# Performance work log

Hardware: AMD Instinct MI355X
Metric: run time of the kernel (lower is better)

The kernel has to match this reference:

```python
import jax, jax.numpy as jnp
import numpy as np

DIM, D_STATE, D_CONV, EXPAND = 1024, 16, 4, 2
D_INNER = EXPAND * DIM
DT_RANK = (DIM + 15) // 16  # 64
B, L = 2, 1024


def setup_inputs() -> dict:
    key = jax.random.key(0)
    ks = jax.random.split(key, 12)
    s = lambda k, shp, sc: jax.random.normal(k, shp, jnp.float32) * sc
    return {
        "x": s(ks[0], (B, L, DIM), 1.0),
        "ln_g": jnp.ones((DIM,), jnp.float32),
        "ln_b": jnp.zeros((DIM,), jnp.float32),
        "W_in": s(ks[1], (DIM, 2 * D_INNER), DIM ** -0.5),
        "conv_w": s(ks[2], (D_INNER, D_CONV), D_CONV ** -0.5),
        "conv_b": jnp.zeros((D_INNER,), jnp.float32),
        "W_x": s(ks[3], (D_INNER, DT_RANK + 2 * D_STATE), D_INNER ** -0.5),
        "W_dt": s(ks[4], (DT_RANK, D_INNER), DT_RANK ** -0.5),
        "b_dt": s(ks[5], (D_INNER,), 0.1),
        "A_log": jnp.log(jnp.broadcast_to(jnp.arange(1, D_STATE + 1, dtype=jnp.float32), (D_INNER, D_STATE))),
        "D_skip": jnp.ones((D_INNER,), jnp.float32),
        "W_out": s(ks[6], (D_INNER, DIM), D_INNER ** -0.5),
    }


def _mamba_block(x, ln_g, ln_b, W_in, conv_w, conv_b, W_x, W_dt, b_dt, A_log, D_skip, W_out):
    # LayerNorm over feature dim
    mu = jnp.mean(x, -1, keepdims=True)
    var = jnp.mean(jnp.square(x - mu), -1, keepdims=True)
    xn = (x - mu) * jax.lax.rsqrt(var + 1e-5) * ln_g + ln_b

    # in_proj -> (u, z), each (B, L, E)
    u, z = jnp.split(xn @ W_in, 2, axis=-1)

    # causal depthwise conv1d over L (kernel D_CONV) + SiLU
    up = jnp.pad(u, ((0, 0), (D_CONV - 1, 0), (0, 0)))
    uc = conv_b
    for k in range(D_CONV):
        uc = uc + conv_w[:, k] * up[:, k:k + L, :]
    uc = jax.nn.silu(uc)

    # input-dependent dt, B, C
    dbl = uc @ W_x
    dt = jax.nn.softplus(dbl[..., :DT_RANK] @ W_dt + b_dt)      # (B,L,E)
    Bc = dbl[..., DT_RANK:DT_RANK + D_STATE]                    # (B,L,N)
    Cc = dbl[..., DT_RANK + D_STATE:]                           # (B,L,N)

    A = -jnp.exp(A_log)                                         # (E,N)
    dA = jnp.exp(dt[..., None] * A)                             # (B,L,E,N)
    dBu = (dt * uc)[..., None] * Bc[:, :, None, :]              # (B,L,E,N)

    # selective scan: h_t = dA_t * h_{t-1} + dBu_t  (associative)
    def comb(c1, c2):
        a1, b1 = c1
        a2, b2 = c2
        return a2 * a1, a2 * b1 + b2

    _, h = jax.lax.associative_scan(comb, (dA, dBu), axis=1)

    y = jnp.einsum('blen,bln->ble', h, Cc) + uc * D_skip
    y = y * jax.nn.silu(z)
    return y @ W_out                                            # (B,L,DIM)


def reference(x, ln_g, ln_b, W_in, conv_w, conv_b, W_x, W_dt, b_dt, A_log, D_skip, W_out):
    return _mamba_block(x, ln_g, ln_b, W_in, conv_w, conv_b, W_x, W_dt, b_dt, A_log, D_skip, W_out)
```

## Files before the change

kernel.cpp:

```cpp
#include <hip/hip_runtime.h>
#include <hip/hip_bf16.h>

typedef __attribute__((ext_vector_type(4))) float  f32x4;
typedef __attribute__((ext_vector_type(8))) __bf16 bf16x8;

typedef __attribute__((address_space(1))) void gvoid_t;
typedef __attribute__((address_space(3))) void lvoid_t;

__device__ __forceinline__ void gld16(const void* g, void* l) {
    __builtin_amdgcn_global_load_lds((const gvoid_t*)g, (lvoid_t*)l, 16, 0, 0);
}

template <int N> __device__ __forceinline__ void vwait() {
    if constexpr (N == 0)      asm volatile("s_waitcnt vmcnt(0)" ::: "memory");
    else if constexpr (N == 6) asm volatile("s_waitcnt vmcnt(6)" ::: "memory");
    else if constexpr (N == 8) asm volatile("s_waitcnt vmcnt(8)" ::: "memory");
}

__device__ __forceinline__ unsigned short f2bf(float f) {
    unsigned u = __builtin_bit_cast(unsigned, f);
    u += 0x7fffu + ((u >> 16) & 1u);
    return (unsigned short)(u >> 16);
}

__device__ __forceinline__ float silu(float x) {
    return x / (1.f + __expf(-x));
}

__global__ __launch_bounds__(256) void k_transpose_cvt(const float* __restrict__ in,
                                                       unsigned short* __restrict__ out,
                                                       int K, int N, int Npad) {
    __shared__ float t[32][33];
    int bn = blockIdx.x * 32;
    int bk = blockIdx.y * 32;
    int c = threadIdx.x & 31, r0 = threadIdx.x >> 5;
    #pragma unroll
    for (int rr = r0; rr < 32; rr += 8) {
        int k = bk + rr, n = bn + c;
        t[rr][c] = (k < K && n < N) ? in[(size_t)k * N + n] : 0.f;
    }
    __syncthreads();
    #pragma unroll
    for (int rr = r0; rr < 32; rr += 8) {
        int n = bn + rr, k = bk + c;
        if (n < Npad && k < K) out[(size_t)n * K + k] = f2bf(t[c][rr]);
    }
}

__global__ __launch_bounds__(256) void k_ln(const float* __restrict__ x,
                                            const float* __restrict__ g,
                                            const float* __restrict__ b,
                                            unsigned short* __restrict__ xn) {
    int row = blockIdx.x;
    const float4* xr = (const float4*)(x + (size_t)row * 1024);
    float4 v = xr[threadIdx.x];
    float s  = v.x + v.y + v.z + v.w;
    float ss = v.x*v.x + v.y*v.y + v.z*v.z + v.w*v.w;
    #pragma unroll
    for (int o = 32; o > 0; o >>= 1) { s += __shfl_down(s, o); ss += __shfl_down(ss, o); }
    __shared__ float red[8];
    if ((threadIdx.x & 63) == 0) { red[threadIdx.x >> 6] = s; red[4 + (threadIdx.x >> 6)] = ss; }
    __syncthreads();
    s  = red[0] + red[1] + red[2] + red[3];
    ss = red[4] + red[5] + red[6] + red[7];
    float mu  = s * (1.f / 1024.f);
    float inv = rsqrtf(ss * (1.f / 1024.f) - mu * mu + 1e-5f);
    float4 gv = ((const float4*)g)[threadIdx.x];
    float4 bv = ((const float4*)b)[threadIdx.x];
    ushort4 o4;
    o4.x = f2bf((v.x - mu) * inv * gv.x + bv.x);
    o4.y = f2bf((v.y - mu) * inv * gv.y + bv.y);
    o4.z = f2bf((v.z - mu) * inv * gv.z + bv.z);
    o4.w = f2bf((v.w - mu) * inv * gv.w + bv.w);
    ((ushort4*)xn)[(size_t)row * 256 + threadIdx.x] = o4;
}

template <int BM, int BN, int EPI>
__global__ __launch_bounds__(256) void k_gemm2(const unsigned short* __restrict__ A,
                                               const unsigned short* __restrict__ Bt,
                                               float* __restrict__ C,
                                               int kchunk, int lda, int ldb, int ldc,
                                               size_t zstride,
                                               const float* __restrict__ bias) {
    constexpr int PA = BM / 32, PB = BN / 32, NV = PA + PB;
    constexpr int MF = BM / 32, NF = BN / 32;
    __shared__ __attribute__((aligned(16))) unsigned short smA[2 * BM * 64];
    __shared__ __attribute__((aligned(16))) unsigned short smB[2 * BN * 64];

    int tid = threadIdx.x, wave = tid >> 6, lane = tid & 63;
    int bm = blockIdx.x * BM, bn = blockIdx.y * BN;
    int kstart = blockIdx.z * kchunk;
    int nt = kchunk >> 6;
    C += (size_t)blockIdx.z * zstride;
    int wm = (wave >> 1) * (BM / 2), wn = (wave & 1) * (BN / 2);
    int lr = lane & 15, lq = lane >> 4;
    int srow = wave * 8 + (lane >> 3);
    int scg  = lane & 7;

    f32x4 acc[MF][NF] = {};

    auto STAGE = [&](int buf, int k0) {
        unsigned short* dA = smA + buf * (BM * 64) + wave * 512;
        unsigned short* dB = smB + buf * (BN * 64) + wave * 512;
        #pragma unroll
        for (int p = 0; p < PA; ++p) {
            int row = p * 32 + srow;
            int gcol = ((scg ^ (row & 7)) << 3) + k0;
            gld16(A + (size_t)(bm + row) * lda + gcol, dA + p * 2048);
        }
        #pragma unroll
        for (int p = 0; p < PB; ++p) {
            int row = p * 32 + srow;
            int gcol = ((scg ^ (row & 7)) << 3) + k0;
            gld16(Bt + (size_t)(bn + row) * ldb + gcol, dB + p * 2048);
        }
    };

    STAGE(0, kstart);
    for (int t = 0; t < nt; ++t) {
        int cur = t & 1;
        if (t + 1 < nt) { STAGE(cur ^ 1, kstart + (t + 1) * 64); vwait<NV>(); }
        else            { vwait<0>(); }
        __builtin_amdgcn_s_barrier();
        const unsigned short* sA = smA + cur * (BM * 64);
        const unsigned short* sB = smB + cur * (BN * 64);
        #pragma unroll
        for (int ks = 0; ks < 2; ++ks) {
            int cg = (ks * 4 + lq) ^ (lr & 7);
            bf16x8 af[MF], bfv[NF];
            #pragma unroll
            for (int i = 0; i < MF; ++i)
                af[i] = *(const bf16x8*)(sA + (wm + i * 16 + lr) * 64 + (cg << 3));
            #pragma unroll
            for (int i = 0; i < NF; ++i)
                bfv[i] = *(const bf16x8*)(sB + (wn + i * 16 + lr) * 64 + (cg << 3));
            #pragma unroll
            for (int mi = 0; mi < MF; ++mi)
                #pragma unroll
                for (int ni = 0; ni < NF; ++ni)
                    acc[mi][ni] = __builtin_amdgcn_mfma_f32_16x16x32_bf16(af[mi], bfv[ni], acc[mi][ni], 0, 0, 0);
        }
        __builtin_amdgcn_s_barrier();
    }

    #pragma unroll
    for (int mi = 0; mi < MF; ++mi) {
        #pragma unroll
        for (int ni = 0; ni < NF; ++ni) {
            int c = bn + wn + ni * 16 + lr;
            #pragma unroll
            for (int v = 0; v < 4; ++v) {
                int r = bm + wm + mi * 16 + (lq << 2) + v;
                float val = acc[mi][ni][v];
                if (EPI == 1) {
                    val += bias[c];
                    val = (val > 20.f) ? val : log1pf(__expf(val));
                }
                C[(size_t)r * ldc + c] = val;
            }
        }
    }
}

__global__ __launch_bounds__(256) void k_red8(const float* __restrict__ part,
                                              float* __restrict__ dbl,
                                              unsigned short* __restrict__ dtr) {
    int idx = blockIdx.x * 256 + threadIdx.x;
    float s = 0.f;
    #pragma unroll
    for (int z = 0; z < 8; ++z) s += part[(size_t)z * 262144 + idx];
    dbl[idx] = s;
    int r = idx >> 7, c = idx & 127;
    if (c < 64) dtr[r * 64 + c] = f2bf(s);
}

__global__ __launch_bounds__(256) void k_conv(const float* __restrict__ uz,
                                              const float* __restrict__ cw,
                                              const float* __restrict__ cb,
                                              float* __restrict__ uc,
                                              unsigned short* __restrict__ ucb) {
    int idx = blockIdx.x * 256 + threadIdx.x;
    int e  = idx & 2047;
    int bl = idx >> 11;
    int l  = bl & 1023;
    float acc = cb[e];
    const float* w = cw + e * 4;
    #pragma unroll
    for (int k = 0; k < 4; ++k) {
        int ls = l - 3 + k;
        if (ls >= 0) acc += w[k] * uz[(size_t)(bl - 3 + k) * 4096 + e];
    }
    float s = silu(acc);
    uc[idx]  = s;
    ucb[idx] = f2bf(s);
}

__global__ __launch_bounds__(256) void k_scan_p1(const float* __restrict__ dt,
                                                 const float* __restrict__ uc,
                                                 const float* __restrict__ dbl,
                                                 const float* __restrict__ A_log,
                                                 float* __restrict__ aggA,
                                                 float* __restrict__ aggH) {
    __shared__ float sBC[64][32];
    int bid = blockIdx.x;
    int c = bid & 15, eblk = (bid >> 4) & 7, b = bid >> 7;
    int t = threadIdx.x;
    int e = eblk * 256 + t;
    int bl0 = b * 1024 + c * 64;
    #pragma unroll
    for (int i = t; i < 512; i += 256) {
        int r = i >> 3, j = i & 7;
        *(float4*)&sBC[r][j * 4] = *(const float4*)(dbl + (size_t)(bl0 + r) * 128 + 64 + j * 4);
    }
    __syncthreads();
    float Aen[16];
    #pragma unroll
    for (int n = 0; n < 16; ++n) Aen[n] = -__expf(A_log[e * 16 + n]);
    bool fastA = true;
    #pragma unroll
    for (int n = 1; n < 16; ++n)
        fastA = fastA && (fabsf(Aen[n] - (n + 1) * Aen[0]) <= 1e-3f);
    float h[16];
    #pragma unroll
    for (int n = 0; n < 16; ++n) h[n] = 0.f;
    float sdt = 0.f;
    size_t idx2 = (size_t)bl0 * 2048 + e;
    #pragma unroll 4
    for (int l = 0; l < 64; ++l) {
        float dtv = dt[idx2], ucv = uc[idx2];
        float dtu = dtv * ucv;
        float dA[16];
        if (fastA) {
            float p = __expf(dtv * Aen[0]);
            float cur = p;
            #pragma unroll
            for (int n = 0; n < 16; ++n) { dA[n] = cur; cur *= p; }
        } else {
            #pragma unroll
            for (int n = 0; n < 16; ++n) dA[n] = __expf(dtv * Aen[n]);
        }
        #pragma unroll
        for (int n = 0; n < 16; ++n)
            h[n] = fmaf(dA[n], h[n], dtu * sBC[l][n]);
        sdt += dtv;
        idx2 += 2048;
    }
    size_t o = ((size_t)(b * 16 + c) * 16) * 2048 + e;
    #pragma unroll
    for (int n = 0; n < 16; ++n) {
        aggA[o + (size_t)n * 2048] = __expf(sdt * Aen[n]);
        aggH[o + (size_t)n * 2048] = h[n];
    }
}

__global__ __launch_bounds__(256) void k_scan_p2(const float* __restrict__ aggA,
                                                 const float* __restrict__ aggH,
                                                 float* __restrict__ hinit) {
    int bid = blockIdx.x;
    int b = bid >> 7, n = (bid >> 3) & 15, eblk = bid & 7;
    int e = eblk * 256 + threadIdx.x;
    float h = 0.f;
    #pragma unroll
    for (int c = 0; c < 16; ++c) {
        size_t base = ((size_t)(b * 16 + c) * 16 + n) * 2048 + e;
        hinit[base] = h;
        h = fmaf(aggA[base], h, aggH[base]);
    }
}

__global__ __launch_bounds__(256) void k_scan_p3(const float* __restrict__ dt,
                                                 const float* __restrict__ uc,
                                                 const float* __restrict__ dbl,
                                                 const float* __restrict__ uz,
                                                 const float* __restrict__ A_log,
                                                 const float* __restrict__ D_skip,
                                                 const float* __restrict__ hinit,
                                                 unsigned short* __restrict__ yg) {
    __shared__ float sBC[64][32];
    int bid = blockIdx.x;
    int c = bid & 15, eblk = (bid >> 4) & 7, b = bid >> 7;
    int t = threadIdx.x;
    int e = eblk * 256 + t;
    int bl0 = b * 1024 + c * 64;
    #pragma unroll
    for (int i = t; i < 512; i += 256) {
        int r = i >> 3, j = i & 7;
        *(float4*)&sBC[r][j * 4] = *(const float4*)(dbl + (size_t)(bl0 + r) * 128 + 64 + j * 4);
    }
    __syncthreads();
    float Aen[16];
    #pragma unroll
    for (int n = 0; n < 16; ++n) Aen[n] = -__expf(A_log[e * 16 + n]);
    bool fastA = true;
    #pragma unroll
    for (int n = 1; n < 16; ++n)
        fastA = fastA && (fabsf(Aen[n] - (n + 1) * Aen[0]) <= 1e-3f);
    float De = D_skip[e];
    size_t o = ((size_t)(b * 16 + c) * 16) * 2048 + e;
    float h[16];
    #pragma unroll
    for (int n = 0; n < 16; ++n) h[n] = hinit[o + (size_t)n * 2048];
    size_t idx2 = (size_t)bl0 * 2048 + e;
    size_t idx4 = (size_t)bl0 * 4096 + 2048 + e;
    #pragma unroll 4
    for (int l = 0; l < 64; ++l) {
        float dtv = dt[idx2], ucv = uc[idx2];
        float zv  = uz[idx4];
        float dtu = dtv * ucv;
        float dA[16];
        if (fastA) {
            float p = __expf(dtv * Aen[0]);
            float cur = p;
            #pragma unroll
            for (int n = 0; n < 16; ++n) { dA[n] = cur; cur *= p; }
        } else {
            #pragma unroll
            for (int n = 0; n < 16; ++n) dA[n] = __expf(dtv * Aen[n]);
        }
        float y = 0.f;
        #pragma unroll
        for (int n = 0; n < 16; ++n) {
            h[n] = fmaf(dA[n], h[n], dtu * sBC[l][n]);
            y = fmaf(h[n], sBC[l][16 + n], y);
        }
        y = (y + ucv * De) * silu(zv);
        yg[idx2] = f2bf(y);
        idx2 += 2048; idx4 += 4096;
    }
}

extern "C" void kernel_launch(void* const* d_in, const int* in_sizes, int n_in,
                              void* d_out, int out_size, void* d_ws, size_t ws_size,
                              hipStream_t stream) {
    const float* x      = (const float*)d_in[0];
    const float* ln_g   = (const float*)d_in[1];
    const float* ln_b   = (const float*)d_in[2];
    const float* W_in   = (const float*)d_in[3];
    const float* conv_w = (const float*)d_in[4];
    const float* conv_b = (const float*)d_in[5];
    const float* W_x    = (const float*)d_in[6];
    const float* W_dt   = (const float*)d_in[7];
    const float* b_dt   = (const float*)d_in[8];
    const float* A_log  = (const float*)d_in[9];
    const float* D_skip = (const float*)d_in[10];
    const float* W_out  = (const float*)d_in[11];
    float* out = (float*)d_out;

    const size_t needed =
        (size_t)4096 * 1024 * 2 + (size_t)1024 * 2048 * 2 + (size_t)2048 * 64 * 2 +
        (size_t)128 * 2048 * 2 + (size_t)2048 * 1024 * 2 + (size_t)2048 * 4096 * 4 +
        (size_t)2048 * 2048 * 4 + (size_t)2048 * 2048 * 2 + (size_t)2048 * 128 * 4 +
        (size_t)2048 * 64 * 2 + (size_t)2048 * 2048 * 4 + (size_t)2048 * 2048 * 2;
    if (ws_size < needed) return;

    char* w = (char*)d_ws;
    unsigned short* WIN_T  = (unsigned short*)w; w += (size_t)4096 * 1024 * 2;
    unsigned short* WOUT_T = (unsigned short*)w; w += (size_t)1024 * 2048 * 2;
    unsigned short* WDT_T  = (unsigned short*)w; w += (size_t)2048 * 64 * 2;
    unsigned short* WX_T   = (unsigned short*)w; w += (size_t)128 * 2048 * 2;
    unsigned short* XN     = (unsigned short*)w; w += (size_t)2048 * 1024 * 2;
    float*          UZ     = (float*)w;          w += (size_t)2048 * 4096 * 4;
    float*          UC     = (float*)w;          w += (size_t)2048 * 2048 * 4;
    unsigned short* UCB    = (unsigned short*)w; w += (size_t)2048 * 2048 * 2;
    float*          DBL    = (float*)w;          w += (size_t)2048 * 128 * 4;
    unsigned short* DTR    = (unsigned short*)w; w += (size_t)2048 * 64 * 2;
    float*          DT     = (float*)w;          w += (size_t)2048 * 2048 * 4;
    unsigned short* YG     = (unsigned short*)w; w += (size_t)2048 * 2048 * 2;

    float* PART  = (float*)WIN_T;
    float* AGGA  = (float*)XN;
    float* AGGH  = (float*)WIN_T;
    float* HINIT = (float*)((char*)WIN_T + (size_t)4 * 1024 * 1024);

    k_transpose_cvt<<<dim3(128, 32), 256, 0, stream>>>(W_in,  WIN_T,  1024, 4096, 4096);
    k_transpose_cvt<<<dim3(32, 64),  256, 0, stream>>>(W_out, WOUT_T, 2048, 1024, 1024);
    k_transpose_cvt<<<dim3(64, 2),   256, 0, stream>>>(W_dt,  WDT_T,  64,   2048, 2048);
    k_transpose_cvt<<<dim3(4, 64),   256, 0, stream>>>(W_x,   WX_T,   2048, 96,   128);

    k_ln<<<2048, 256, 0, stream>>>(x, ln_g, ln_b, XN);

    k_gemm2<128, 128, 0><<<dim3(16, 32, 1), 256, 0, stream>>>(XN, WIN_T, UZ, 1024, 1024, 1024, 4096, 0, nullptr);

    k_conv<<<16384, 256, 0, stream>>>(UZ, conv_w, conv_b, UC, UCB);

    k_gemm2<64, 128, 0><<<dim3(32, 1, 8), 256, 0, stream>>>(UCB, WX_T, PART, 256, 2048, 2048, 128, (size_t)2048 * 128, nullptr);
    k_red8<<<1024, 256, 0, stream>>>(PART, DBL, DTR);

    k_gemm2<128, 128, 1><<<dim3(16, 16, 1), 256, 0, stream>>>(DTR, WDT_T, DT, 64, 64, 64, 2048, 0, b_dt);

    k_scan_p1<<<256, 256, 0, stream>>>(DT, UC, DBL, A_log, AGGA, AGGH);
    k_scan_p2<<<256, 256, 0, stream>>>(AGGA, AGGH, HINIT);
    k_scan_p3<<<256, 256, 0, stream>>>(DT, UC, DBL, UZ, A_log, D_skip, HINIT, YG);

    k_gemm2<64, 128, 0><<<dim3(32, 8, 1), 256, 0, stream>>>(YG, WOUT_T, out, 2048, 2048, 2048, 1024, 0, nullptr);
}
```

Baseline: 285.0 us.

## Fuse prep kernels, split in_proj epilogue, recompute conv in scan, drop scan pass 2

Merges the four weight transpose/convert launches and LayerNorm into one k_prep launch. The in_proj GEMM epilogue now writes u as fp32 and silu(z) as bf16, which removes the fp32 z round trip. The scan kernels recompute the causal conv plus SiLU from u instead of reading a stored fp32 uc. The separate chunk-carry pass is folded into scan pass 3, which rebuilds the initial state serially from per-chunk aggH and summed dt. This cuts launches and memory traffic, but pass 3 now does up to 15 extra serial chunk combines per thread, and z is kept in bf16.

```diff
diff --git a/kernel.cpp b/kernel.cpp
--- a/kernel.cpp
+++ b/kernel.cpp
@@ -22,17 +22,19 @@
     u += 0x7fffu + ((u >> 16) & 1u);
     return (unsigned short)(u >> 16);
 }
-
+__device__ __forceinline__ float bf2f(unsigned short u) {
+    return __builtin_bit_cast(float, (unsigned)u << 16);
+}
 __device__ __forceinline__ float silu(float x) {
     return x / (1.f + __expf(-x));
 }
 
-__global__ __launch_bounds__(256) void k_transpose_cvt(const float* __restrict__ in,
-                                                       unsigned short* __restrict__ out,
-                                                       int K, int N, int Npad) {
-    __shared__ float t[32][33];
-    int bn = blockIdx.x * 32;
-    int bk = blockIdx.y * 32;
+__device__ __forceinline__ void tr_cvt(const float* __restrict__ in,
+                                       unsigned short* __restrict__ out,
+                                       int K, int N, int Npad, int bnb, int bkb,
+                                       float* sh) {
+    float (*t)[33] = (float(*)[33])sh;
+    int bn = bnb * 32, bk = bkb * 32;
     int c = threadIdx.x & 31, r0 = threadIdx.x >> 5;
     #pragma unroll
     for (int rr = r0; rr < 32; rr += 8) {
@@ -47,38 +49,54 @@
     }
 }
 
-__global__ __launch_bounds__(256) void k_ln(const float* __restrict__ x,
-                                            const float* __restrict__ g,
-                                            const float* __restrict__ b,
-                                            unsigned short* __restrict__ xn) {
-    int row = blockIdx.x;
-    const float4* xr = (const float4*)(x + (size_t)row * 1024);
-    float4 v = xr[threadIdx.x];
-    float s  = v.x + v.y + v.z + v.w;
-    float ss = v.x*v.x + v.y*v.y + v.z*v.z + v.w*v.w;
-    #pragma unroll
-    for (int o = 32; o > 0; o >>= 1) { s += __shfl_down(s, o); ss += __shfl_down(ss, o); }
-    __shared__ float red[8];
-    if ((threadIdx.x & 63) == 0) { red[threadIdx.x >> 6] = s; red[4 + (threadIdx.x >> 6)] = ss; }
-    __syncthreads();
-    s  = red[0] + red[1] + red[2] + red[3];
-    ss = red[4] + red[5] + red[6] + red[7];
-    float mu  = s * (1.f / 1024.f);
-    float inv = rsqrtf(ss * (1.f / 1024.f) - mu * mu + 1e-5f);
-    float4 gv = ((const float4*)g)[threadIdx.x];
-    float4 bv = ((const float4*)b)[threadIdx.x];
-    ushort4 o4;
-    o4.x = f2bf((v.x - mu) * inv * gv.x + bv.x);
-    o4.y = f2bf((v.y - mu) * inv * gv.y + bv.y);
-    o4.z = f2bf((v.z - mu) * inv * gv.z + bv.z);
-    o4.w = f2bf((v.w - mu) * inv * gv.w + bv.w);
-    ((ushort4*)xn)[(size_t)row * 256 + threadIdx.x] = o4;
+__global__ __launch_bounds__(256) void k_prep(const float* __restrict__ x,
+                                              const float* __restrict__ g,
+                                              const float* __restrict__ b,
+                                              unsigned short* __restrict__ xn,
+                                              const float* __restrict__ W_in,  unsigned short* __restrict__ WIN_T,
+                                              const float* __restrict__ W_out, unsigned short* __restrict__ WOUT_T,
+                                              const float* __restrict__ W_dt,  unsigned short* __restrict__ WDT_T,
+                                              const float* __restrict__ W_x,   unsigned short* __restrict__ WX_T) {
+    __shared__ float sh[32 * 33];
+    int bid = blockIdx.x;
+    if (bid < 2048) {
+        int row = bid;
+        const float4* xr = (const float4*)(x + (size_t)row * 1024);
+        float4 v = xr[threadIdx.x];
+        float s  = v.x + v.y + v.z + v.w;
+        float ss = v.x*v.x + v.y*v.y + v.z*v.z + v.w*v.w;
+        #pragma unroll
+        for (int o = 32; o > 0; o >>= 1) { s += __shfl_down(s, o); ss += __shfl_down(ss, o); }
+        if ((threadIdx.x & 63) == 0) { sh[threadIdx.x >> 6] = s; sh[4 + (threadIdx.x >> 6)] = ss; }
+        __syncthreads();
+        s  = sh[0] + sh[1] + sh[2] + sh[3];
+        ss = sh[4] + sh[5] + sh[6] + sh[7];
+        float mu  = s * (1.f / 1024.f);
+        float inv = rsqrtf(ss * (1.f / 1024.f) - mu * mu + 1e-5f);
+        float4 gv = ((const float4*)g)[threadIdx.x];
+        float4 bv = ((const float4*)b)[threadIdx.x];
+        ushort4 o4;
+        o4.x = f2bf((v.x - mu) * inv * gv.x + bv.x);
+        o4.y = f2bf((v.y - mu) * inv * gv.y + bv.y);
+        o4.z = f2bf((v.z - mu) * inv * gv.z + bv.z);
+        o4.w = f2bf((v.w - mu) * inv * gv.w + bv.w);
+        ((ushort4*)xn)[(size_t)row * 256 + threadIdx.x] = o4;
+    } else if (bid < 6144) {
+        int i = bid - 2048;  tr_cvt(W_in,  WIN_T,  1024, 4096, 4096, i & 127, i >> 7, sh);
+    } else if (bid < 8192) {
+        int i = bid - 6144;  tr_cvt(W_out, WOUT_T, 2048, 1024, 1024, i & 31,  i >> 5, sh);
+    } else if (bid < 8320) {
+        int i = bid - 8192;  tr_cvt(W_dt,  WDT_T,  64,   2048, 2048, i & 63,  i >> 6, sh);
+    } else {
+        int i = bid - 8320;  tr_cvt(W_x,   WX_T,   2048, 96,   128,  i & 3,   i >> 2, sh);
+    }
 }
 
 template <int BM, int BN, int EPI>
 __global__ __launch_bounds__(256) void k_gemm2(const unsigned short* __restrict__ A,
                                                const unsigned short* __restrict__ Bt,
                                                float* __restrict__ C,
+                                               unsigned short* __restrict__ C2,
                                                int kchunk, int lda, int ldb, int ldc,
                                                size_t zstride,
                                                const float* __restrict__ bias) {
@@ -152,11 +170,16 @@
             for (int v = 0; v < 4; ++v) {
                 int r = bm + wm + mi * 16 + (lq << 2) + v;
                 float val = acc[mi][ni][v];
-                if (EPI == 1) {
+                if (EPI == 0) {
+                    C[(size_t)r * ldc + c] = val;
+                } else if (EPI == 1) {
                     val += bias[c];
                     val = (val > 20.f) ? val : log1pf(__expf(val));
+                    C[(size_t)r * ldc + c] = val;
+                } else {
+                    if (c < 2048) C[(size_t)r * 2048 + c] = val;
+                    else          C2[(size_t)r * 2048 + (c - 2048)] = f2bf(silu(val));
                 }
-                C[(size_t)r * ldc + c] = val;
             }
         }
     }
@@ -174,43 +197,43 @@
     if (c < 64) dtr[r * 64 + c] = f2bf(s);
 }
 
-__global__ __launch_bounds__(256) void k_conv(const float* __restrict__ uz,
-                                              const float* __restrict__ cw,
-                                              const float* __restrict__ cb,
-                                              float* __restrict__ uc,
-                                              unsigned short* __restrict__ ucb) {
+__global__ __launch_bounds__(256) void k_conv2(const float* __restrict__ U,
+                                               const float* __restrict__ cw,
+                                               const float* __restrict__ cb,
+                                               unsigned short* __restrict__ ucb) {
     int idx = blockIdx.x * 256 + threadIdx.x;
     int e  = idx & 2047;
     int bl = idx >> 11;
     int l  = bl & 1023;
     float acc = cb[e];
-    const float* w = cw + e * 4;
+    float4 wv = *(const float4*)(cw + e * 4);
+    float w4[4] = {wv.x, wv.y, wv.z, wv.w};
     #pragma unroll
     for (int k = 0; k < 4; ++k) {
         int ls = l - 3 + k;
-        if (ls >= 0) acc += w[k] * uz[(size_t)(bl - 3 + k) * 4096 + e];
-    }
-    float s = silu(acc);
-    uc[idx]  = s;
-    ucb[idx] = f2bf(s);
-}
-
-__global__ __launch_bounds__(256) void k_scan_p1(const float* __restrict__ dt,
-                                                 const float* __restrict__ uc,
+        if (ls >= 0) acc += w4[k] * U[(size_t)(bl - 3 + k) * 2048 + e];
+    }
+    ucb[idx] = f2bf(silu(acc));
+}
+
+
+__global__ __launch_bounds__(256) void k_scan_p1(const float* __restrict__ U,
+                                                 const float* __restrict__ dt,
                                                  const float* __restrict__ dbl,
                                                  const float* __restrict__ A_log,
-                                                 float* __restrict__ aggA,
-                                                 float* __restrict__ aggH) {
-    __shared__ float sBC[64][32];
+                                                 const float* __restrict__ cw,
+                                                 const float* __restrict__ cb,
+                                                 float* __restrict__ aggH,
+                                                 float* __restrict__ sdtb) {
+    __shared__ float sB[64][16];
     int bid = blockIdx.x;
     int c = bid & 15, eblk = (bid >> 4) & 7, b = bid >> 7;
     int t = threadIdx.x;
     int e = eblk * 256 + t;
     int bl0 = b * 1024 + c * 64;
-    #pragma unroll
-    for (int i = t; i < 512; i += 256) {
-        int r = i >> 3, j = i & 7;
-        *(float4*)&sBC[r][j * 4] = *(const float4*)(dbl + (size_t)(bl0 + r) * 128 + 64 + j * 4);
+    {
+        int r = t >> 2, j4 = t & 3;
+        *(float4*)&sB[r][j4 * 4] = *(const float4*)(dbl + (size_t)(bl0 + r) * 128 + 64 + j4 * 4);
     }
     __syncthreads();
     float Aen[16];
@@ -220,14 +243,25 @@
     #pragma unroll
     for (int n = 1; n < 16; ++n)
         fastA = fastA && (fabsf(Aen[n] - (n + 1) * Aen[0]) <= 1e-3f);
+    float4 wv = *(const float4*)(cw + e * 4);
+    float cbv = cb[e];
+    float um3 = 0.f, um2 = 0.f, um1 = 0.f;
+    if (c > 0) {
+        um3 = U[(size_t)(bl0 - 3) * 2048 + e];
+        um2 = U[(size_t)(bl0 - 2) * 2048 + e];
+        um1 = U[(size_t)(bl0 - 1) * 2048 + e];
+    }
     float h[16];
     #pragma unroll
     for (int n = 0; n < 16; ++n) h[n] = 0.f;
     float sdt = 0.f;
-    size_t idx2 = (size_t)bl0 * 2048 + e;
+    size_t iu = (size_t)bl0 * 2048 + e;
     #pragma unroll 4
     for (int l = 0; l < 64; ++l) {
-        float dtv = dt[idx2], ucv = uc[idx2];
+        float u0  = U[iu];
+        float dtv = dt[iu];
+        float ucv = silu(cbv + wv.x * um3 + wv.y * um2 + wv.z * um1 + wv.w * u0);
+        um3 = um2; um2 = um1; um1 = u0;
         float dtu = dtv * ucv;
         float dA[16];
         if (fastA) {
@@ -241,40 +275,26 @@
         }
         #pragma unroll
         for (int n = 0; n < 16; ++n)
-            h[n] = fmaf(dA[n], h[n], dtu * sBC[l][n]);
+            h[n] = fmaf(dA[n], h[n], dtu * sB[l][n]);
         sdt += dtv;
-        idx2 += 2048;
+        iu += 2048;
     }
     size_t o = ((size_t)(b * 16 + c) * 16) * 2048 + e;
     #pragma unroll
-    for (int n = 0; n < 16; ++n) {
-        aggA[o + (size_t)n * 2048] = __expf(sdt * Aen[n]);
-        aggH[o + (size_t)n * 2048] = h[n];
-    }
-}
-
-__global__ __launch_bounds__(256) void k_scan_p2(const float* __restrict__ aggA,
-                                                 const float* __restrict__ aggH,
-                                                 float* __restrict__ hinit) {
-    int bid = blockIdx.x;
-    int b = bid >> 7, n = (bid >> 3) & 15, eblk = bid & 7;
-    int e = eblk * 256 + threadIdx.x;
-    float h = 0.f;
-    #pragma unroll
-    for (int c = 0; c < 16; ++c) {
-        size_t base = ((size_t)(b * 16 + c) * 16 + n) * 2048 + e;
-        hinit[base] = h;
-        h = fmaf(aggA[base], h, aggH[base]);
-    }
-}
-
-__global__ __launch_bounds__(256) void k_scan_p3(const float* __restrict__ dt,
-                                                 const float* __restrict__ uc,
+    for (int n = 0; n < 16; ++n) aggH[o + (size_t)n * 2048] = h[n];
+    sdtb[(size_t)(b * 16 + c) * 2048 + e] = sdt;
+}
+
+__global__ __launch_bounds__(256) void k_scan_p3(const float* __restrict__ U,
+                                                 const float* __restrict__ dt,
                                                  const float* __restrict__ dbl,
-                                                 const float* __restrict__ uz,
+                                                 const unsigned short* __restrict__ sz,
                                                  const float* __restrict__ A_log,
                                                  const float* __restrict__ D_skip,
-                                                 const float* __restrict__ hinit,
+                                                 const float* __restrict__ cw,
+                                                 const float* __restrict__ cb,
+                                                 const float* __restrict__ aggH,
+                                                 const float* __restrict__ sdtb,
                                                  unsigned short* __restrict__ yg) {
     __shared__ float sBC[64][32];
     int bid = blockIdx.x;
@@ -296,16 +316,42 @@
     for (int n = 1; n < 16; ++n)
         fastA = fastA && (fabsf(Aen[n] - (n + 1) * Aen[0]) <= 1e-3f);
     float De = D_skip[e];
-    size_t o = ((size_t)(b * 16 + c) * 16) * 2048 + e;
+    float4 wv = *(const float4*)(cw + e * 4);
+    float cbv = cb[e];
     float h[16];
     #pragma unroll
-    for (int n = 0; n < 16; ++n) h[n] = hinit[o + (size_t)n * 2048];
-    size_t idx2 = (size_t)bl0 * 2048 + e;
-    size_t idx4 = (size_t)bl0 * 4096 + 2048 + e;
+    for (int n = 0; n < 16; ++n) h[n] = 0.f;
+    for (int cc = 0; cc < c; ++cc) {
+        float sdtc = sdtb[(size_t)(b * 16 + cc) * 2048 + e];
+        size_t oa = ((size_t)(b * 16 + cc) * 16) * 2048 + e;
+        float aa[16];
+        if (fastA) {
+            float p = __expf(sdtc * Aen[0]);
+            float cur = p;
+            #pragma unroll
+            for (int n = 0; n < 16; ++n) { aa[n] = cur; cur *= p; }
+        } else {
+            #pragma unroll
+            for (int n = 0; n < 16; ++n) aa[n] = __expf(sdtc * Aen[n]);
+        }
+        #pragma unroll
+        for (int n = 0; n < 16; ++n)
+            h[n] = fmaf(aa[n], h[n], aggH[oa + (size_t)n * 2048]);
+    }
+    float um3 = 0.f, um2 = 0.f, um1 = 0.f;
+    if (c > 0) {
+        um3 = U[(size_t)(bl0 - 3) * 2048 + e];
+        um2 = U[(size_t)(bl0 - 2) * 2048 + e];
+        um1 = U[(size_t)(bl0 - 1) * 2048 + e];
+    }
+    size_t iu = (size_t)bl0 * 2048 + e;
     #pragma unroll 4
     for (int l = 0; l < 64; ++l) {
-        float dtv = dt[idx2], ucv = uc[idx2];
-        float zv  = uz[idx4];
+        float u0  = U[iu];
+        float dtv = dt[iu];
+        float szv = bf2f(sz[iu]);
+        float ucv = silu(cbv + wv.x * um3 + wv.y * um2 + wv.z * um1 + wv.w * u0);
+        um3 = um2; um2 = um1; um1 = u0;
         float dtu = dtv * ucv;
         float dA[16];
         if (fastA) {
@@ -323,9 +369,9 @@
             h[n] = fmaf(dA[n], h[n], dtu * sBC[l][n]);
             y = fmaf(h[n], sBC[l][16 + n], y);
         }
-        y = (y + ucv * De) * silu(zv);
-        yg[idx2] = f2bf(y);
-        idx2 += 2048; idx4 += 4096;
+        y = (y + ucv * De) * szv;
+        yg[iu] = f2bf(y);
+        iu += 2048;
     }
 }
 
@@ -359,38 +405,35 @@
     unsigned short* WDT_T  = (unsigned short*)w; w += (size_t)2048 * 64 * 2;
     unsigned short* WX_T   = (unsigned short*)w; w += (size_t)128 * 2048 * 2;
     unsigned short* XN     = (unsigned short*)w; w += (size_t)2048 * 1024 * 2;
-    float*          UZ     = (float*)w;          w += (size_t)2048 * 4096 * 4;
-    float*          UC     = (float*)w;          w += (size_t)2048 * 2048 * 4;
+    float*          U      = (float*)w;          w += (size_t)2048 * 2048 * 4;
+    unsigned short* SZ     = (unsigned short*)w; w += (size_t)2048 * 2048 * 2;
+    w += (size_t)2048 * 2048 * 2;
     unsigned short* UCB    = (unsigned short*)w; w += (size_t)2048 * 2048 * 2;
+    w += (size_t)2048 * 2048 * 2 + (size_t)2048 * 2048 * 2;
     float*          DBL    = (float*)w;          w += (size_t)2048 * 128 * 4;
     unsigned short* DTR    = (unsigned short*)w; w += (size_t)2048 * 64 * 2;
     float*          DT     = (float*)w;          w += (size_t)2048 * 2048 * 4;
     unsigned short* YG     = (unsigned short*)w; w += (size_t)2048 * 2048 * 2;
 
-    float* PART  = (float*)WIN_T;
-    float* AGGA  = (float*)XN;
-    float* AGGH  = (float*)WIN_T;
-    float* HINIT = (float*)((char*)WIN_T + (size_t)4 * 1024 * 1024);
-
-    k_transpose_cvt<<<dim3(128, 32), 256, 0, stream>>>(W_in,  WIN_T,  1024, 4096, 4096);
-    k_transpose_cvt<<<dim3(32, 64),  256, 0, stream>>>(W_out, WOUT_T, 2048, 1024, 1024);
-    k_transpose_cvt<<<dim3(64, 2),   256, 0, stream>>>(W_dt,  WDT_T,  64,   2048, 2048);
-    k_transpose_cvt<<<dim3(4, 64),   256, 0, stream>>>(W_x,   WX_T,   2048, 96,   128);
-
-    k_ln<<<2048, 256, 0, stream>>>(x, ln_g, ln_b, XN);
-
-    k_gemm2<128, 128, 0><<<dim3(16, 32, 1), 256, 0, stream>>>(XN, WIN_T, UZ, 1024, 1024, 1024, 4096, 0, nullptr);
-
-    k_conv<<<16384, 256, 0, stream>>>(UZ, conv_w, conv_b, UC, UCB);
-
-    k_gemm2<64, 128, 0><<<dim3(32, 1, 8), 256, 0, stream>>>(UCB, WX_T, PART, 256, 2048, 2048, 128, (size_t)2048 * 128, nullptr);
+    float* PART = (float*)WIN_T;
+    float* SDT  = (float*)WIN_T;
+    float* AGGH = (float*)XN;
+
+    k_prep<<<8576, 256, 0, stream>>>(x, ln_g, ln_b, XN,
+                                     W_in, WIN_T, W_out, WOUT_T, W_dt, WDT_T, W_x, WX_T);
+
+    k_gemm2<128, 128, 2><<<dim3(16, 32, 1), 256, 0, stream>>>(XN, WIN_T, U, SZ, 1024, 1024, 1024, 2048, 0, nullptr);
+
+    k_conv2<<<16384, 256, 0, stream>>>(U, conv_w, conv_b, UCB);
+
+    k_gemm2<64, 128, 0><<<dim3(32, 1, 8), 256, 0, stream>>>(UCB, WX_T, PART, nullptr, 256, 2048, 2048, 128, (size_t)2048 * 128, nullptr);
+
     k_red8<<<1024, 256, 0, stream>>>(PART, DBL, DTR);
 
-    k_gemm2<128, 128, 1><<<dim3(16, 16, 1), 256, 0, stream>>>(DTR, WDT_T, DT, 64, 64, 64, 2048, 0, b_dt);
-
-    k_scan_p1<<<256, 256, 0, stream>>>(DT, UC, DBL, A_log, AGGA, AGGH);
-    k_scan_p2<<<256, 256, 0, stream>>>(AGGA, AGGH, HINIT);
-    k_scan_p3<<<256, 256, 0, stream>>>(DT, UC, DBL, UZ, A_log, D_skip, HINIT, YG);
-
-    k_gemm2<64, 128, 0><<<dim3(32, 8, 1), 256, 0, stream>>>(YG, WOUT_T, out, 2048, 2048, 2048, 1024, 0, nullptr);
-}
+    k_gemm2<128, 128, 1><<<dim3(16, 16, 1), 256, 0, stream>>>(DTR, WDT_T, DT, nullptr, 64, 64, 64, 2048, 0, b_dt);
+
+    k_scan_p1<<<256, 256, 0, stream>>>(U, DT, DBL, A_log, conv_w, conv_b, AGGH, SDT);
+    k_scan_p3<<<256, 256, 0, stream>>>(U, DT, DBL, SZ, A_log, D_skip, conv_w, conv_b, AGGH, SDT, YG);
+
+    k_gemm2<64, 128, 0><<<dim3(32, 8, 1), 256, 0, stream>>>(YG, WOUT_T, out, nullptr, 2048, 2048, 2048, 1024, 0, nullptr);
+}
```

New measurement: 283.4 us. About the same (-0.6%).
